# Kernel tuning notes

Hardware: AMD Instinct MI355X
Metric: run time of the kernel (lower is better)

The kernel has to match this reference:

```python
import jax, jax.numpy as jnp
import numpy as np

D_MODEL = 1024
NUM_HEADS = 16
D_K = D_MODEL // NUM_HEADS
THETA = 10000.0
B, T = 2, 2048


def _rope(x, pos, theta):
    # x: [B, H, T, d_k]; pos: [T] int. Rotates consecutive pairs (2x2 rotation blocks),
    # matching rearrange '... t (s d2) -> ... t s d2' with d2=2 in the original.
    d = x.shape[-1]
    j = jnp.arange(d // 2, dtype=x.dtype)
    ang = pos.astype(x.dtype)[:, None] / (theta ** (2.0 * j / d))  # [T, d/2]
    cos, sin = jnp.cos(ang), jnp.sin(ang)
    x1, x2 = x[..., 0::2], x[..., 1::2]
    out1 = cos * x1 - sin * x2
    out2 = sin * x1 + cos * x2
    return jnp.stack([out1, out2], axis=-1).reshape(x.shape)


def setup_inputs() -> dict:
    key = jax.random.key(0)
    ks = jax.random.split(key, 5)
    std = 2.0 / (D_MODEL + D_MODEL)
    return {
        "x": jax.random.normal(ks[0], (B, T, D_MODEL), dtype=jnp.float32),
        "token_positions": jnp.arange(T, dtype=jnp.int64),
        "Wq": jax.random.normal(ks[1], (D_MODEL, D_MODEL), dtype=jnp.float32) * std,
        "Wk": jax.random.normal(ks[2], (D_MODEL, D_MODEL), dtype=jnp.float32) * std,
        "Wv": jax.random.normal(ks[3], (D_MODEL, D_MODEL), dtype=jnp.float32) * std,
        "Wo": jax.random.normal(ks[4], (D_MODEL, D_MODEL), dtype=jnp.float32) * std,
    }


def reference(x, token_positions, Wq, Wk, Wv, Wo):
    b, t, d = x.shape
    # Linear: einsum('out in, ... in -> ... out') == x @ W.T
    q = jnp.einsum('btd,ed->bte', x, Wq)
    k = jnp.einsum('btd,ed->bte', x, Wk)
    v = jnp.einsum('btd,ed->bte', x, Wv)
    # split heads -> [B, H, T, d_k]
    q = q.reshape(b, t, NUM_HEADS, D_K).transpose(0, 2, 1, 3)
    k = k.reshape(b, t, NUM_HEADS, D_K).transpose(0, 2, 1, 3)
    v = v.reshape(b, t, NUM_HEADS, D_K).transpose(0, 2, 1, 3)
    q = _rope(q, token_positions, THETA)
    k = _rope(k, token_positions, THETA)
    scores = jnp.einsum('bhqd,bhkd->bhqk', q, k) / jnp.sqrt(jnp.asarray(D_K, x.dtype))
    causal = jnp.tril(jnp.ones((t, t), dtype=bool))
    scores = jnp.where(causal, scores, -jnp.inf)
    attn = jax.nn.softmax(scores, axis=-1)
    out = jnp.einsum('bhqk,bhkd->bhqd', attn, v)  # [B,H,T,d_k]
    out = out.transpose(0, 2, 1, 3).reshape(b, t, d)
    return jnp.einsum('bte,de->btd', out, Wo)
```

## Files before the change

kernel.cpp:

```cpp
#include <hip/hip_runtime.h>
#include <hip/hip_bf16.h>
#include <math.h>

#define BATCH 2
#define SEQ 2048
#define DM 1024
#define NH 16
#define DK 64
#define KDIM 1024

typedef __bf16 bf16_t;
typedef __bf16 bf16x4 __attribute__((ext_vector_type(4)));
typedef __bf16 bf16x8 __attribute__((ext_vector_type(8)));
typedef float floatx4 __attribute__((ext_vector_type(4)));

typedef __attribute__((address_space(3))) void lds_void;
typedef __attribute__((address_space(1))) const void gbl_void;

__global__ __launch_bounds__(256) void cast_all(
    const float* __restrict__ x, const float* __restrict__ wq,
    const float* __restrict__ wk, const float* __restrict__ wv,
    const float* __restrict__ wo,
    bf16_t* __restrict__ xb, bf16_t* __restrict__ wqkb,
    bf16_t* __restrict__ wvb, bf16_t* __restrict__ wob) {
  int i = blockIdx.x * blockDim.x + threadIdx.x;
  const int R0 = 1 << 20, RW = 1 << 18;
  const float* src; bf16_t* dst; int off;
  if (i < R0)                { src = x;  dst = xb;              off = i; }
  else if (i < R0 + RW)      { src = wq; dst = wqkb;            off = i - R0; }
  else if (i < R0 + 2 * RW)  { src = wk; dst = wqkb + (1 << 20); off = i - R0 - RW; }
  else if (i < R0 + 3 * RW)  { src = wv; dst = wvb;             off = i - R0 - 2 * RW; }
  else                       { src = wo; dst = wob;             off = i - R0 - 3 * RW; }
  float4 f = *(const float4*)(src + (size_t)off * 4);
  bf16x4 v = {(bf16_t)f.x, (bf16_t)f.y, (bf16_t)f.z, (bf16_t)f.w};
  *(bf16x4*)(dst + (size_t)off * 4) = v;
}

template <int TM>
__device__ __forceinline__ void gemm_body(
    const bf16_t* __restrict__ A, const bf16_t* __restrict__ B,
    void* __restrict__ out0, void* __restrict__ out1, int mode,
    int bi, int bj) {
  constexpr int MFR = TM / 32;
  constexpr int AINST = (TM * 4) / 256;
  __shared__ bf16_t As[2][TM * 32];
  __shared__ bf16_t Bs[2][128 * 32];

  const int tid = threadIdx.x;
  const int lane = tid & 63;
  const int w = tid >> 6;
  const int quad = lane >> 4;
  const int l16 = lane & 15;
  const int wi = w >> 1, wj = w & 1;
  const int i0 = bi * TM;
  const int j0 = bj * 128;

  const bf16_t* gA[AINST]; const bf16_t* gB[2];
  int lAo[AINST], lBo[2];
#pragma unroll
  for (int jj = 0; jj < AINST; ++jj) {
    int s = jj * 256 + tid;
    int r = s >> 2;
    int c = (s & 3) ^ ((r >> 1) & 3);
    gA[jj] = A + (size_t)(i0 + r) * KDIM + c * 8;
    lAo[jj] = (jj * 256 + (tid & ~63)) * 8;
  }
#pragma unroll
  for (int jj = 0; jj < 2; ++jj) {
    int s = jj * 256 + tid;
    int r = s >> 2;
    int c = (s & 3) ^ ((r >> 1) & 3);
    gB[jj] = B + (size_t)(j0 + r) * KDIM + c * 8;
    lBo[jj] = (jj * 256 + (tid & ~63)) * 8;
  }

  int offA[MFR], offB[4];
#pragma unroll
  for (int mi = 0; mi < MFR; ++mi) {
    int rowA = wi * (TM / 2) + mi * 16 + l16;
    offA[mi] = (rowA * 4 + (quad ^ ((rowA >> 1) & 3))) * 8;
  }
#pragma unroll
  for (int nj = 0; nj < 4; ++nj) {
    int rowB = wj * 64 + nj * 16 + l16;
    offB[nj] = (rowB * 4 + (quad ^ ((rowB >> 1) & 3))) * 8;
  }

  floatx4 acc[MFR][4];
#pragma unroll
  for (int a = 0; a < MFR; ++a)
#pragma unroll
    for (int b = 0; b < 4; ++b) acc[a][b] = (floatx4){0.f, 0.f, 0.f, 0.f};

#pragma unroll
  for (int jj = 0; jj < AINST; ++jj)
    __builtin_amdgcn_global_load_lds((gbl_void*)gA[jj],
                                     (lds_void*)(As[0] + lAo[jj]), 16, 0, 0);
#pragma unroll
  for (int jj = 0; jj < 2; ++jj)
    __builtin_amdgcn_global_load_lds((gbl_void*)gB[jj],
                                     (lds_void*)(Bs[0] + lBo[jj]), 16, 0, 0);

  const int NK = KDIM / 32;
  for (int kt = 0; kt < NK; ++kt) {
    const int cur = kt & 1;
    __syncthreads();
    if (kt + 1 < NK) {
      const size_t koff = (size_t)(kt + 1) * 32;
#pragma unroll
      for (int jj = 0; jj < AINST; ++jj)
        __builtin_amdgcn_global_load_lds((gbl_void*)(gA[jj] + koff),
                                         (lds_void*)(As[cur ^ 1] + lAo[jj]), 16, 0, 0);
#pragma unroll
      for (int jj = 0; jj < 2; ++jj)
        __builtin_amdgcn_global_load_lds((gbl_void*)(gB[jj] + koff),
                                         (lds_void*)(Bs[cur ^ 1] + lBo[jj]), 16, 0, 0);
    }
    bf16x8 af[MFR], bfr[4];
#pragma unroll
    for (int mi = 0; mi < MFR; ++mi) af[mi] = *(const bf16x8*)&As[cur][offA[mi]];
#pragma unroll
    for (int nj = 0; nj < 4; ++nj) bfr[nj] = *(const bf16x8*)&Bs[cur][offB[nj]];
#pragma unroll
    for (int mi = 0; mi < MFR; ++mi)
#pragma unroll
      for (int nj = 0; nj < 4; ++nj)
        acc[mi][nj] = __builtin_amdgcn_mfma_f32_16x16x32_bf16(
            af[mi], bfr[nj], acc[mi][nj], 0, 0, 0);
  }

  const float L2T_32 = 13.2877123795494f / 32.0f;
#pragma unroll
  for (int mi = 0; mi < MFR; ++mi) {
    int ib = i0 + wi * (TM / 2) + mi * 16 + quad * 4;
#pragma unroll
    for (int nj = 0; nj < 4; ++nj) {
      int jb = j0 + wj * 64 + nj * 16 + l16;
      floatx4 v = acc[mi][nj];
      if (mode == 0) {
        int tok = jb, b = tok >> 11, t = tok & (SEQ - 1);
        int e = ib;
        int h = (e >> 6) & (NH - 1), dk = e & 63;
        int jp = dk >> 1;
        float s0, c0, s1, c1;
        sincosf((float)t * exp2f(-(float)jp * L2T_32), &s0, &c0);
        sincosf((float)t * exp2f(-(float)(jp + 1) * L2T_32), &s1, &c1);
        bf16x4 sv = {(bf16_t)(c0 * v[0] - s0 * v[1]),
                     (bf16_t)(s0 * v[0] + c0 * v[1]),
                     (bf16_t)(c1 * v[2] - s1 * v[3]),
                     (bf16_t)(s1 * v[2] + c1 * v[3])};
        bf16_t* dst = (bf16_t*)(e < DM ? out0 : out1);
        *(bf16x4*)(dst + (((size_t)(b * NH + h)) * SEQ + t) * DK + dk) = sv;
      } else if (mode == 1) {
        bf16x4 sv = {(bf16_t)v[0], (bf16_t)v[1], (bf16_t)v[2], (bf16_t)v[3]};
        *(bf16x4*)((bf16_t*)out0 + (size_t)jb * (BATCH * SEQ) + ib) = sv;
      } else {
        *(floatx4*)((float*)out0 + (size_t)jb * DM + ib) = v;
      }
    }
  }
}

__global__ __launch_bounds__(256) void gemm_qkv(
    const bf16_t* __restrict__ wqkb, const bf16_t* __restrict__ wvb,
    const bf16_t* __restrict__ xb,
    bf16_t* __restrict__ qb, bf16_t* __restrict__ kb,
    bf16_t* __restrict__ vtb) {
  const int bid = blockIdx.x;
  const bf16_t *A, *B; void *o0, *o1 = nullptr; int mode, bi, bj;
  if (bid < 512) {
    A = wqkb; B = xb; o0 = qb; o1 = kb; mode = 0;
    int x = bid & 7, s = bid >> 3;
    bi = (x & 1) * 8 + (s & 7);
    bj = (x >> 1) * 8 + (s >> 3);
  } else {
    int r = bid - 512;
    A = xb; B = wvb; o0 = vtb; mode = 1;
    int x = r & 7, s = r >> 3;
    bi = (x & 3) * 8 + (s & 7);
    bj = (x >> 2) * 4 + (s >> 3);
  }
  gemm_body<128>(A, B, o0, o1, mode, bi, bj);
}

__global__ __launch_bounds__(256) void gemm_out(
    const bf16_t* __restrict__ wob, const bf16_t* __restrict__ ab,
    float* __restrict__ out) {
  const int bid = blockIdx.x;
  int x = bid & 7, s = bid >> 3;
  int bi = (x & 1) * 8 + (s & 7);
  int bj = (x >> 1) * 8 + (s >> 3);
  gemm_body<64>(wob, ab, out, nullptr, 2, bi, bj);
}

__global__ __launch_bounds__(256) void attn_mfma(
    const bf16_t* __restrict__ Q, const bf16_t* __restrict__ K,
    const bf16_t* __restrict__ Vt, bf16_t* __restrict__ Out) {
  __shared__ bf16_t Ks[128 * 64];
  __shared__ bf16_t Vs[64 * 128];
  __shared__ bf16_t Ps[4][32][72];
  __shared__ float  Lw[4][2][16];

  const int tid = threadIdx.x;
  const int lane = tid & 63;
  const int w = tid >> 6;
  const int quad = lane >> 4;
  const int l16 = lane & 15;

  const int id = blockIdx.x;
  const int bh = id & 31;
  const int b = bh >> 4;
  const int h = bh & 15;
  const int g = id >> 5;
  const int qt = (g < 8) ? g : 23 - g;
  const int q0 = qt * 128;

  const bf16_t* Qb = Q + ((size_t)bh * SEQ + q0) * DK;
  const bf16_t* Kb = K + (size_t)bh * SEQ * DK;
  const bf16_t* Vb = Vt + (size_t)(h * DK) * (BATCH * SEQ) + (size_t)b * SEQ;

  bf16x8 qa[2][2];
#pragma unroll
  for (int qs = 0; qs < 2; ++qs) {
    const bf16_t* qrow = Qb + (size_t)(w * 32 + qs * 16 + l16) * DK;
    qa[qs][0] = *(const bf16x8*)(qrow + quad * 8);
    qa[qs][1] = *(const bf16x8*)(qrow + 32 + quad * 8);
  }

  const bf16_t* gk[4]; const bf16_t* gv[4];
  bf16_t* lk[4]; bf16_t* lv[4];
#pragma unroll
  for (int i = 0; i < 4; ++i) {
    int s = (w * 4 + i) * 64 + lane;
    int rK = s >> 3, cK = (s & 7) ^ (rK & 7);
    gk[i] = Kb + (size_t)rK * DK + cK * 8;
    lk[i] = Ks + (size_t)s * 8;
    int rV = s >> 4, cV = (s & 15) ^ (rV & 15);
    gv[i] = Vb + (size_t)rV * (BATCH * SEQ) + cV * 8;
    lv[i] = Vs + (size_t)s * 8;
  }

  floatx4 o[2][4];
#pragma unroll
  for (int qs = 0; qs < 2; ++qs)
#pragma unroll
    for (int nt = 0; nt < 4; ++nt) o[qs][nt] = (floatx4){0.f, 0.f, 0.f, 0.f};
  float l_part[2] = {0.f, 0.f};

  const int l7 = l16 & 7;
  const int ntiles = qt + 1;
  for (int kt = 0; kt < ntiles; ++kt) {
    __syncthreads();
#pragma unroll
    for (int i = 0; i < 4; ++i) {
      __builtin_amdgcn_global_load_lds((gbl_void*)(gk[i] + (size_t)kt * 128 * DK),
                                       (lds_void*)lk[i], 16, 0, 0);
      __builtin_amdgcn_global_load_lds((gbl_void*)(gv[i] + (size_t)kt * 128),
                                       (lds_void*)lv[i], 16, 0, 0);
    }
    __syncthreads();

    const bool diag = (kt == qt);
#pragma unroll
    for (int hunk = 0; hunk < 2; ++hunk) {
#pragma unroll
      for (int ntl = 0; ntl < 4; ++ntl) {
        const int nt = hunk * 4 + ntl;
        const int rowK = nt * 16 + l16;
        bf16x8 ka0 = *(const bf16x8*)&Ks[rowK * 64 + ((quad ^ l7) * 8)];
        bf16x8 ka1 = *(const bf16x8*)&Ks[rowK * 64 + (((4 + quad) ^ l7) * 8)];
#pragma unroll
        for (int qs = 0; qs < 2; ++qs) {
          floatx4 st = {0.f, 0.f, 0.f, 0.f};
          st = __builtin_amdgcn_mfma_f32_16x16x32_bf16(ka0, qa[qs][0], st, 0, 0, 0);
          st = __builtin_amdgcn_mfma_f32_16x16x32_bf16(ka1, qa[qs][1], st, 0, 0, 0);
          const int kvbase = kt * 128 + nt * 16 + quad * 4;
          const int qcol = q0 + w * 32 + qs * 16 + l16;
          float p[4];
#pragma unroll
          for (int r = 0; r < 4; ++r) {
            float e = __expf(st[r] * 0.125f);
            if (diag) e = (kvbase + r <= qcol) ? e : 0.f;
            p[r] = e;
            l_part[qs] += e;
          }
          bf16x4 pk = {(bf16_t)p[0], (bf16_t)p[1], (bf16_t)p[2], (bf16_t)p[3]};
          *(bf16x4*)&Ps[w][qs * 16 + l16][ntl * 16 + quad * 4] = pk;
        }
      }
      bf16x8 pa[2][2];
#pragma unroll
      for (int qs = 0; qs < 2; ++qs)
#pragma unroll
        for (int ksl = 0; ksl < 2; ++ksl)
          pa[qs][ksl] = *(const bf16x8*)&Ps[w][qs * 16 + l16][ksl * 32 + quad * 8];
#pragma unroll
      for (int ntp = 0; ntp < 4; ++ntp) {
        const int rowV = ntp * 16 + l16;
#pragma unroll
        for (int ksl = 0; ksl < 2; ++ksl) {
          const int ks = hunk * 2 + ksl;
          bf16x8 vb = *(const bf16x8*)&Vs[rowV * 128 + (((4 * ks + quad) ^ l16) * 8)];
#pragma unroll
          for (int qs = 0; qs < 2; ++qs)
            o[qs][ntp] = __builtin_amdgcn_mfma_f32_16x16x32_bf16(
                pa[qs][ksl], vb, o[qs][ntp], 0, 0, 0);
        }
      }
    }
  }

#pragma unroll
  for (int qs = 0; qs < 2; ++qs) {
    float l = l_part[qs];
    l += __shfl_xor(l, 16, 64);
    l += __shfl_xor(l, 32, 64);
    if (quad == 0) Lw[w][qs][l16] = l;
  }
#pragma unroll
  for (int qs = 0; qs < 2; ++qs) {
    float4 lv4 = *(const float4*)&Lw[w][qs][quad * 4];
    float inv[4] = {1.f / lv4.x, 1.f / lv4.y, 1.f / lv4.z, 1.f / lv4.w};
#pragma unroll
    for (int r = 0; r < 4; ++r) {
      int t = q0 + w * 32 + qs * 16 + quad * 4 + r;
      bf16_t* orow = Out + ((size_t)b * SEQ + t) * DM + h * DK;
#pragma unroll
      for (int ntp = 0; ntp < 4; ++ntp)
        orow[ntp * 16 + l16] = (bf16_t)(o[qs][ntp][r] * inv[r]);
    }
  }
}

extern "C" void kernel_launch(void* const* d_in, const int* in_sizes, int n_in,
                              void* d_out, int out_size, void* d_ws, size_t ws_size,
                              hipStream_t stream) {
  const float* x  = (const float*)d_in[0];
  const float* Wq = (const float*)d_in[2];
  const float* Wk = (const float*)d_in[3];
  const float* Wv = (const float*)d_in[4];
  const float* Wo = (const float*)d_in[5];
  float* out = (float*)d_out;

  const size_t M1 = (size_t)1024 * 1024;
  bf16_t* xb   = (bf16_t*)d_ws;
  bf16_t* wqkb = xb + 4 * M1;
  bf16_t* wvb  = wqkb + 2 * M1;
  bf16_t* wob  = wvb + M1;
  bf16_t* qb   = wob + M1;
  bf16_t* kb   = qb + 4 * M1;
  bf16_t* vtb  = kb + 4 * M1;
  bf16_t* ab   = vtb + 4 * M1;

  cast_all<<<8192, 256, 0, stream>>>(x, Wq, Wk, Wv, Wo, xb, wqkb, wvb, wob);
  gemm_qkv<<<768, 256, 0, stream>>>(wqkb, wvb, xb, qb, kb, vtb);
  attn_mfma<<<512, 256, 0, stream>>>(qb, kb, vtb, ab);
  gemm_out<<<512, 256, 0, stream>>>(wob, ab, out);
}
```

Baseline: 193.0 us.

## Use 32x32x16 MFMA in GEMMs and precompute RoPE sin/cos table

The shared GEMM body moves from 16x16x32 bf16 MFMA tiles to 32x32x16 tiles with 16-wide accumulators, and the LDS fragment addressing and epilogue indexing are reworked to match. RoPE cos/sin values are computed once per (position, pair) in extra blocks of the cast kernel and written to a workspace table, which the QKV epilogue then reads instead of calling sincosf/exp2f per element. The aim is higher MFMA throughput with fewer LDS reads per flop, and a cheaper epilogue. The cost is an extra table in global memory plus table loads in the epilogue, and the cast kernel now has to finish before gemm_qkv can use the table.

```diff
diff --git a/kernel.cpp b/kernel.cpp
--- a/kernel.cpp
+++ b/kernel.cpp
@@ -13,6 +13,7 @@
 typedef __bf16 bf16x4 __attribute__((ext_vector_type(4)));
 typedef __bf16 bf16x8 __attribute__((ext_vector_type(8)));
 typedef float floatx4 __attribute__((ext_vector_type(4)));
+typedef float floatx16 __attribute__((ext_vector_type(16)));
 
 typedef __attribute__((address_space(3))) void lds_void;
 typedef __attribute__((address_space(1))) const void gbl_void;
@@ -22,9 +23,20 @@
     const float* __restrict__ wk, const float* __restrict__ wv,
     const float* __restrict__ wo,
     bf16_t* __restrict__ xb, bf16_t* __restrict__ wqkb,
-    bf16_t* __restrict__ wvb, bf16_t* __restrict__ wob) {
+    bf16_t* __restrict__ wvb, bf16_t* __restrict__ wob,
+    float* __restrict__ rope_tab) {
   int i = blockIdx.x * blockDim.x + threadIdx.x;
   const int R0 = 1 << 20, RW = 1 << 18;
+  const int TOT = R0 + 4 * RW;
+  if (i >= TOT) {
+    int idx = i - TOT;
+    int t = idx >> 5, jp = idx & 31;
+    const float L2T_32 = 13.2877123795494f / 32.0f;
+    float s, c;
+    sincosf((float)t * exp2f(-(float)jp * L2T_32), &s, &c);
+    *(float2*)(rope_tab + (size_t)idx * 2) = make_float2(c, s);
+    return;
+  }
   const float* src; bf16_t* dst; int off;
   if (i < R0)                { src = x;  dst = xb;              off = i; }
   else if (i < R0 + RW)      { src = wq; dst = wqkb;            off = i - R0; }
@@ -39,9 +51,10 @@
 template <int TM>
 __device__ __forceinline__ void gemm_body(
     const bf16_t* __restrict__ A, const bf16_t* __restrict__ B,
+    const float* __restrict__ rope_tab,
     void* __restrict__ out0, void* __restrict__ out1, int mode,
     int bi, int bj) {
-  constexpr int MFR = TM / 32;
+  constexpr int MFR2 = TM / 64;
   constexpr int AINST = (TM * 4) / 256;
   __shared__ bf16_t As[2][TM * 32];
   __shared__ bf16_t Bs[2][128 * 32];
@@ -49,8 +62,8 @@
   const int tid = threadIdx.x;
   const int lane = tid & 63;
   const int w = tid >> 6;
-  const int quad = lane >> 4;
-  const int l16 = lane & 15;
+  const int l32 = lane & 31;
+  const int khalf = lane >> 5;
   const int wi = w >> 1, wj = w & 1;
   const int i0 = bi * TM;
   const int j0 = bj * 128;
@@ -74,23 +87,33 @@
     lBo[jj] = (jj * 256 + (tid & ~63)) * 8;
   }
 
-  int offA[MFR], offB[4];
-#pragma unroll
-  for (int mi = 0; mi < MFR; ++mi) {
-    int rowA = wi * (TM / 2) + mi * 16 + l16;
-    offA[mi] = (rowA * 4 + (quad ^ ((rowA >> 1) & 3))) * 8;
-  }
-#pragma unroll
-  for (int nj = 0; nj < 4; ++nj) {
-    int rowB = wj * 64 + nj * 16 + l16;
-    offB[nj] = (rowB * 4 + (quad ^ ((rowB >> 1) & 3))) * 8;
-  }
-
-  floatx4 acc[MFR][4];
-#pragma unroll
-  for (int a = 0; a < MFR; ++a)
-#pragma unroll
-    for (int b = 0; b < 4; ++b) acc[a][b] = (floatx4){0.f, 0.f, 0.f, 0.f};
+  int offA[MFR2][2], offB[2][2];
+#pragma unroll
+  for (int ti = 0; ti < MFR2; ++ti) {
+    int row = wi * (TM / 2) + ti * 32 + l32;
+#pragma unroll
+    for (int s = 0; s < 2; ++s) {
+      int c = s * 2 + khalf;
+      offA[ti][s] = (row * 4 + (c ^ ((row >> 1) & 3))) * 8;
+    }
+  }
+#pragma unroll
+  for (int tj = 0; tj < 2; ++tj) {
+    int row = wj * 64 + tj * 32 + l32;
+#pragma unroll
+    for (int s = 0; s < 2; ++s) {
+      int c = s * 2 + khalf;
+      offB[tj][s] = (row * 4 + (c ^ ((row >> 1) & 3))) * 8;
+    }
+  }
+
+  floatx16 acc[MFR2][2];
+#pragma unroll
+  for (int a = 0; a < MFR2; ++a)
+#pragma unroll
+    for (int b = 0; b < 2; ++b)
+#pragma unroll
+      for (int e = 0; e < 16; ++e) acc[a][b][e] = 0.f;
 
 #pragma unroll
   for (int jj = 0; jj < AINST; ++jj)
@@ -116,46 +139,63 @@
         __builtin_amdgcn_global_load_lds((gbl_void*)(gB[jj] + koff),
                                          (lds_void*)(Bs[cur ^ 1] + lBo[jj]), 16, 0, 0);
     }
-    bf16x8 af[MFR], bfr[4];
-#pragma unroll
-    for (int mi = 0; mi < MFR; ++mi) af[mi] = *(const bf16x8*)&As[cur][offA[mi]];
-#pragma unroll
-    for (int nj = 0; nj < 4; ++nj) bfr[nj] = *(const bf16x8*)&Bs[cur][offB[nj]];
-#pragma unroll
-    for (int mi = 0; mi < MFR; ++mi)
-#pragma unroll
-      for (int nj = 0; nj < 4; ++nj)
-        acc[mi][nj] = __builtin_amdgcn_mfma_f32_16x16x32_bf16(
-            af[mi], bfr[nj], acc[mi][nj], 0, 0, 0);
-  }
-
-  const float L2T_32 = 13.2877123795494f / 32.0f;
-#pragma unroll
-  for (int mi = 0; mi < MFR; ++mi) {
-    int ib = i0 + wi * (TM / 2) + mi * 16 + quad * 4;
-#pragma unroll
-    for (int nj = 0; nj < 4; ++nj) {
-      int jb = j0 + wj * 64 + nj * 16 + l16;
-      floatx4 v = acc[mi][nj];
+    bf16x8 af[MFR2][2], bfr[2][2];
+#pragma unroll
+    for (int ti = 0; ti < MFR2; ++ti)
+#pragma unroll
+      for (int s = 0; s < 2; ++s) af[ti][s] = *(const bf16x8*)&As[cur][offA[ti][s]];
+#pragma unroll
+    for (int tj = 0; tj < 2; ++tj)
+#pragma unroll
+      for (int s = 0; s < 2; ++s) bfr[tj][s] = *(const bf16x8*)&Bs[cur][offB[tj][s]];
+#pragma unroll
+    for (int s = 0; s < 2; ++s)
+#pragma unroll
+      for (int ti = 0; ti < MFR2; ++ti)
+#pragma unroll
+        for (int tj = 0; tj < 2; ++tj)
+          acc[ti][tj] = __builtin_amdgcn_mfma_f32_32x32x16_bf16(
+              af[ti][s], bfr[tj][s], acc[ti][tj], 0, 0, 0);
+  }
+
+#pragma unroll
+  for (int ti = 0; ti < MFR2; ++ti) {
+#pragma unroll
+    for (int tj = 0; tj < 2; ++tj) {
+      const int jb = j0 + wj * 64 + tj * 32 + l32;
+      floatx16 a16 = acc[ti][tj];
       if (mode == 0) {
-        int tok = jb, b = tok >> 11, t = tok & (SEQ - 1);
-        int e = ib;
-        int h = (e >> 6) & (NH - 1), dk = e & 63;
-        int jp = dk >> 1;
-        float s0, c0, s1, c1;
-        sincosf((float)t * exp2f(-(float)jp * L2T_32), &s0, &c0);
-        sincosf((float)t * exp2f(-(float)(jp + 1) * L2T_32), &s1, &c1);
-        bf16x4 sv = {(bf16_t)(c0 * v[0] - s0 * v[1]),
-                     (bf16_t)(s0 * v[0] + c0 * v[1]),
-                     (bf16_t)(c1 * v[2] - s1 * v[3]),
-                     (bf16_t)(s1 * v[2] + c1 * v[3])};
-        bf16_t* dst = (bf16_t*)(e < DM ? out0 : out1);
-        *(bf16x4*)(dst + (((size_t)(b * NH + h)) * SEQ + t) * DK + dk) = sv;
+        const int bidx = jb >> 11, t = jb & (SEQ - 1);
+#pragma unroll
+        for (int g = 0; g < 4; ++g) {
+          int e = i0 + wi * (TM / 2) + ti * 32 + 8 * g + 4 * khalf;
+          int h = (e >> 6) & (NH - 1), dk = e & 63;
+          int jp = dk >> 1;
+          float4 cs = *(const float4*)(rope_tab + ((size_t)t * 32 + jp) * 2);
+          float v0 = a16[4 * g], v1 = a16[4 * g + 1];
+          float v2 = a16[4 * g + 2], v3 = a16[4 * g + 3];
+          bf16x4 sv = {(bf16_t)(cs.x * v0 - cs.y * v1),
+                       (bf16_t)(cs.y * v0 + cs.x * v1),
+                       (bf16_t)(cs.z * v2 - cs.w * v3),
+                       (bf16_t)(cs.w * v2 + cs.z * v3)};
+          bf16_t* dst = (bf16_t*)(e < DM ? out0 : out1);
+          *(bf16x4*)(dst + (((size_t)(bidx * NH + h)) * SEQ + t) * DK + dk) = sv;
+        }
       } else if (mode == 1) {
-        bf16x4 sv = {(bf16_t)v[0], (bf16_t)v[1], (bf16_t)v[2], (bf16_t)v[3]};
-        *(bf16x4*)((bf16_t*)out0 + (size_t)jb * (BATCH * SEQ) + ib) = sv;
+#pragma unroll
+        for (int g = 0; g < 4; ++g) {
+          int ib = i0 + wi * (TM / 2) + ti * 32 + 8 * g + 4 * khalf;
+          bf16x4 sv = {(bf16_t)a16[4 * g], (bf16_t)a16[4 * g + 1],
+                       (bf16_t)a16[4 * g + 2], (bf16_t)a16[4 * g + 3]};
+          *(bf16x4*)((bf16_t*)out0 + (size_t)jb * (BATCH * SEQ) + ib) = sv;
+        }
       } else {
-        *(floatx4*)((float*)out0 + (size_t)jb * DM + ib) = v;
+#pragma unroll
+        for (int g = 0; g < 4; ++g) {
+          int ib = i0 + wi * (TM / 2) + ti * 32 + 8 * g + 4 * khalf;
+          floatx4 v4 = {a16[4 * g], a16[4 * g + 1], a16[4 * g + 2], a16[4 * g + 3]};
+          *(floatx4*)((float*)out0 + (size_t)jb * DM + ib) = v4;
+        }
       }
     }
   }
@@ -163,7 +203,7 @@
 
 __global__ __launch_bounds__(256) void gemm_qkv(
     const bf16_t* __restrict__ wqkb, const bf16_t* __restrict__ wvb,
-    const bf16_t* __restrict__ xb,
+    const bf16_t* __restrict__ xb, const float* __restrict__ rope_tab,
     bf16_t* __restrict__ qb, bf16_t* __restrict__ kb,
     bf16_t* __restrict__ vtb) {
   const int bid = blockIdx.x;
@@ -180,7 +220,7 @@
     bi = (x & 3) * 8 + (s & 7);
     bj = (x >> 2) * 4 + (s >> 3);
   }
-  gemm_body<128>(A, B, o0, o1, mode, bi, bj);
+  gemm_body<128>(A, B, rope_tab, o0, o1, mode, bi, bj);
 }
 
 __global__ __launch_bounds__(256) void gemm_out(
@@ -190,7 +230,7 @@
   int x = bid & 7, s = bid >> 3;
   int bi = (x & 1) * 8 + (s & 7);
   int bj = (x >> 1) * 8 + (s >> 3);
-  gemm_body<64>(wob, ab, out, nullptr, 2, bi, bj);
+  gemm_body<64>(wob, ab, nullptr, out, nullptr, 2, bi, bj);
 }
 
 __global__ __launch_bounds__(256) void attn_mfma(
@@ -351,9 +391,11 @@
   bf16_t* kb   = qb + 4 * M1;
   bf16_t* vtb  = kb + 4 * M1;
   bf16_t* ab   = vtb + 4 * M1;
-
-  cast_all<<<8192, 256, 0, stream>>>(x, Wq, Wk, Wv, Wo, xb, wqkb, wvb, wob);
-  gemm_qkv<<<768, 256, 0, stream>>>(wqkb, wvb, xb, qb, kb, vtb);
+  float* rope_tab = (float*)(ab + 4 * M1);
+
+  cast_all<<<8448, 256, 0, stream>>>(x, Wq, Wk, Wv, Wo, xb, wqkb, wvb, wob,
+                                     rope_tab);
+  gemm_qkv<<<768, 256, 0, stream>>>(wqkb, wvb, xb, rope_tab, qb, kb, vtb);
   attn_mfma<<<512, 256, 0, stream>>>(qb, kb, vtb, ab);
   gemm_out<<<512, 256, 0, stream>>>(wob, ab, out);
 }
```

Result: no change. 196.1 us (+1.6%).
